# Performance work log

Measured on AMD Instinct MI355X. Metric: run time of the kernel, lower is better.

Reference implementation:

```python
import jax, jax.numpy as jnp
import numpy as np

B, T, C, H = 4, 2048, 1024, 16
HS = C // H  # 64
THRESH_INIT = (5 + 1) / 12 * 0.01  # (layer_idx+1)/n_layer * final_token_threshold


def _layernorm(x, w, b, eps=1e-5):
    mu = jnp.mean(x, axis=-1, keepdims=True)
    var = jnp.var(x, axis=-1, keepdims=True)
    return (x - mu) * jax.lax.rsqrt(var + eps) * w + b


def setup_inputs() -> dict:
    key = jax.random.key(0)
    ks = jax.random.split(key, 8)
    s = 0.02
    inp = {
        'x': jax.random.normal(ks[0], (B, T, C), dtype=jnp.float32),
        'attention_mask': jnp.ones((B, T), dtype=jnp.float32),
        'protected_mask': jnp.zeros((B, T), dtype=jnp.float32),
        'ln1_w': jnp.ones((C,), jnp.float32),
        'ln1_b': jnp.zeros((C,), jnp.float32),
        'c_attn_w': jax.random.normal(ks[1], (3 * C, C), jnp.float32) * s,
        'c_attn_b': jnp.zeros((3 * C,), jnp.float32),
        'c_proj_w': jax.random.normal(ks[2], (C, C), jnp.float32) * s,
        'c_proj_b': jnp.zeros((C,), jnp.float32),
        'ln2_w': jnp.ones((C,), jnp.float32),
        'ln2_b': jnp.zeros((C,), jnp.float32),
        'fc_w': jax.random.normal(ks[3], (4 * C, C), jnp.float32) * s,
        'fc_b': jnp.zeros((4 * C,), jnp.float32),
        'fcproj_w': jax.random.normal(ks[4], (C, 4 * C), jnp.float32) * s,
        'fcproj_b': jnp.zeros((C,), jnp.float32),
        'threshold': jnp.asarray(THRESH_INIT, jnp.float32),
    }
    return inp


def reference(x, attention_mask, protected_mask, ln1_w, ln1_b, c_attn_w, c_attn_b,
              c_proj_w, c_proj_b, ln2_w, ln2_b, fc_w, fc_b, fcproj_w, fcproj_b, threshold):
    b, t, c = x.shape
    # --- attention with importance scores ---
    h = _layernorm(x, ln1_w, ln1_b)
    qkv = h @ c_attn_w.T + c_attn_b                      # (B,T,3C)
    q, k, v = jnp.split(qkv, 3, axis=-1)
    q = q.reshape(b, t, H, HS).transpose(0, 2, 1, 3)     # (B,H,T,hs)
    k = k.reshape(b, t, H, HS).transpose(0, 2, 1, 3)
    v = v.reshape(b, t, H, HS).transpose(0, 2, 1, 3)
    att = jnp.einsum('bhqd,bhkd->bhqk', q, k) / np.sqrt(HS)
    causal = jnp.tril(jnp.ones((t, t), dtype=bool))      # (T,T)
    att = jnp.where(causal[None, None], att, -jnp.inf)
    att = jnp.where(attention_mask[:, None, None, :] != 0, att, -jnp.inf)
    att = jax.nn.softmax(att, axis=-1)                   # (B,H,T,T)
    y = jnp.einsum('bhqk,bhkd->bhqd', att, v)
    y = y.transpose(0, 2, 1, 3).reshape(b, t, c)
    y = y @ c_proj_w.T + c_proj_b
    importance = att.mean(axis=1).mean(axis=1)           # (B,T): mean over heads, then queries
    # --- pruning ---
    x = x + y
    pruning_mask = (importance >= threshold).astype(x.dtype)  # hard mode
    pruning_mask = jnp.where(protected_mask > 0, jnp.ones_like(pruning_mask), pruning_mask)
    combined_mask = attention_mask * pruning_mask
    x = x * combined_mask[..., None]
    # --- MLP ---
    m = _layernorm(x, ln2_w, ln2_b)
    m = jax.nn.gelu(m @ fc_w.T + fc_b, approximate=False)
    x = x + (m @ fcproj_w.T + fcproj_b)
    pruning_loss = jnp.asarray(0.0, x.dtype)  # hard mode / lambda=0
    return (x, combined_mask, pruning_loss)
```

## Files before the change

kernel.cpp:

```cpp
#include <hip/hip_runtime.h>
#include <math.h>

#define B_ 4
#define T_ 2048
#define C_ 1024
#define H_ 16
#define NROWS (B_*T_)

typedef short s8v  __attribute__((ext_vector_type(8)));
typedef float f4v  __attribute__((ext_vector_type(4)));
typedef unsigned short u16v4 __attribute__((ext_vector_type(4)));

static __device__ __forceinline__ unsigned short f2bf(float x) {
    unsigned u = __float_as_uint(x);
    unsigned r = u + 0x7fffu + ((u >> 16) & 1u);
    return (unsigned short)(r >> 16);
}

static __device__ __forceinline__ void gload_lds16(const void* g, void* l) {
    __builtin_amdgcn_global_load_lds(
        (const __attribute__((address_space(1))) void*)g,
        (__attribute__((address_space(3))) void*)l, 16, 0, 0);
}

__global__ __launch_bounds__(256) void ln_bf16(const float* __restrict__ x,
        const float* __restrict__ w, const float* __restrict__ b,
        unsigned short* __restrict__ out, const int* __restrict__ flag)
{
    if (flag && flag[0] == 0) return;
    int row = blockIdx.x;
    int tid = threadIdx.x;
    const float4* xr = (const float4*)(x + (size_t)row * C_);
    float4 v = xr[tid];
    float s  = v.x + v.y + v.z + v.w;
    float ss = v.x*v.x + v.y*v.y + v.z*v.z + v.w*v.w;
    #pragma unroll
    for (int off = 32; off > 0; off >>= 1) {
        s  += __shfl_down(s,  off, 64);
        ss += __shfl_down(ss, off, 64);
    }
    __shared__ float rs[4], rss[4];
    __shared__ float smu, srstd;
    int wave = tid >> 6, lane = tid & 63;
    if (lane == 0) { rs[wave] = s; rss[wave] = ss; }
    __syncthreads();
    if (tid == 0) {
        float S  = rs[0]+rs[1]+rs[2]+rs[3];
        float SS = rss[0]+rss[1]+rss[2]+rss[3];
        float mu = S * (1.0f/C_);
        float var = SS * (1.0f/C_) - mu*mu;
        smu = mu; srstd = rsqrtf(var + 1e-5f);
    }
    __syncthreads();
    float mu = smu, rstd = srstd;
    float4 wv = ((const float4*)w)[tid];
    float4 bv = ((const float4*)b)[tid];
    u16v4 o;
    o.x = f2bf((v.x-mu)*rstd*wv.x + bv.x);
    o.y = f2bf((v.y-mu)*rstd*wv.y + bv.y);
    o.z = f2bf((v.z-mu)*rstd*wv.z + bv.z);
    o.w = f2bf((v.w-mu)*rstd*wv.w + bv.w);
    *(u16v4*)(out + (size_t)row * C_ + tid*4) = o;
}

__global__ __launch_bounds__(256) void cvt_bf16(const float* __restrict__ in,
        unsigned short* __restrict__ out, int n4, const int* __restrict__ flag)
{
    if (flag && flag[0] == 0) return;
    int i = blockIdx.x * 256 + threadIdx.x;
    if (i < n4) {
        float4 v = ((const float4*)in)[i];
        u16v4 o = { f2bf(v.x), f2bf(v.y), f2bf(v.z), f2bf(v.w) };
        *(u16v4*)(out + (size_t)i*4) = o;
    }
}

__global__ __launch_bounds__(256) void cvt3_bf16(
        const float* __restrict__ cprojw, const float* __restrict__ fcw,
        const float* __restrict__ fcpw,
        unsigned short* __restrict__ wproj, unsigned short* __restrict__ wfc,
        unsigned short* __restrict__ wfcp, const int* __restrict__ flag)
{
    if (flag[0] == 0) return;
    int i = blockIdx.x * 256 + threadIdx.x;
    const int n1 = C_*C_/4;
    const int n2 = n1 + C_*C_;
    const float* src; unsigned short* dst; int j;
    if (i < n1)      { src = cprojw; dst = wproj; j = i; }
    else if (i < n2) { src = fcw;    dst = wfc;   j = i - n1; }
    else             { src = fcpw;   dst = wfcp;  j = i - n2; }
    float4 v = ((const float4*)src)[j];
    u16v4 o = { f2bf(v.x), f2bf(v.y), f2bf(v.z), f2bf(v.w) };
    *(u16v4*)(dst + (size_t)j*4) = o;
}

__global__ void zero_kernel(float* p, int n) {
    int i = blockIdx.x * 256 + threadIdx.x;
    if (i < n) p[i] = 0.f;
}

template<int EPI>
__global__ __launch_bounds__(256) void gemm_bf16(
    const unsigned short* __restrict__ A,
    const unsigned short* __restrict__ Bw,
    const float* __restrict__ bias,
    const float* __restrict__ res,
    float* __restrict__ Cout, unsigned short* __restrict__ Cbf,
    int K, int lda, int ldb, int ldc, int ncoff,
    const float* __restrict__ cmv,
    unsigned short* __restrict__ qh, unsigned short* __restrict__ kh,
    unsigned short* __restrict__ vh, const int* __restrict__ flag)
{
    if (flag && flag[0] == 0) return;
    __shared__ unsigned short As[128*64];
    __shared__ unsigned short Bs[128*64];
    int tid = threadIdx.x;
    int w = tid >> 6, lane = tid & 63, quad = lane >> 4, l16 = lane & 15;
    int wr = w >> 1, wc = w & 1;
    int m0 = blockIdx.y * 128, n0 = blockIdx.x * 128;

    size_t offA[4], offB[4];
    #pragma unroll
    for (int j = 0; j < 4; j++) {
        int ci = j*256 + tid;
        int mr = ci >> 3, kcs = ci & 7;
        int kc = kcs ^ (mr & 7);
        offA[j] = (size_t)(m0 + mr) * lda + kc*8;
        offB[j] = (size_t)(n0 + mr) * ldb + kc*8;
    }

    f4v acc[4][4];
    #pragma unroll
    for (int i = 0; i < 4; i++)
        #pragma unroll
        for (int j = 0; j < 4; j++) { acc[i][j][0]=0.f; acc[i][j][1]=0.f; acc[i][j][2]=0.f; acc[i][j][3]=0.f; }

    for (int k0 = 0; k0 < K; k0 += 64) {
        __syncthreads();
        #pragma unroll
        for (int j = 0; j < 4; j++) {
            gload_lds16(A  + offA[j] + k0, &As[(j*256 + (w<<6))*8]);
            gload_lds16(Bw + offB[j] + k0, &Bs[(j*256 + (w<<6))*8]);
        }
        __syncthreads();
        #pragma unroll
        for (int c = 0; c < 2; c++) {
            s8v af[4], bf[4];
            int sw = ((c<<2) + quad) ^ (l16 & 7);
            #pragma unroll
            for (int i = 0; i < 4; i++) {
                int mr = wr*64 + i*16 + l16;
                af[i] = *(const s8v*)&As[mr*64 + sw*8];
                int nr = wc*64 + i*16 + l16;
                bf[i] = *(const s8v*)&Bs[nr*64 + sw*8];
            }
            #pragma unroll
            for (int i = 0; i < 4; i++)
                #pragma unroll
                for (int j = 0; j < 4; j++)
                    acc[i][j] = __builtin_amdgcn_mfma_f32_16x16x32_bf16(af[i], bf[j], acc[i][j], 0, 0, 0);
        }
    }

    #pragma unroll
    for (int j = 0; j < 4; j++) {
        int ncol = n0 + wc*64 + j*16 + l16;
        float bv = bias ? bias[ncol] : 0.f;
        int hh = 0, dd = 0;
        bool qsec = false;
        unsigned short* basep = nullptr;
        if (EPI == 3) {
            int ncolg = ncol + ncoff;
            int sec = ncolg >> 10;
            int hn = ncolg & 1023;
            hh = hn >> 6; dd = hn & 63;
            basep = (sec == 0) ? qh : (sec == 1) ? kh : vh;
            qsec = (sec == 0);
        }
        #pragma unroll
        for (int i = 0; i < 4; i++) {
            #pragma unroll
            for (int reg = 0; reg < 4; reg++) {
                int m = m0 + wr*64 + i*16 + quad*4 + reg;
                float v = acc[i][j][reg] + bv;
                if (EPI == 1) {
                    v = 0.5f * v * (1.0f + erff(v * 0.70710678118654752f));
                    Cbf[(size_t)m*ldc + ncol] = f2bf(v);
                } else if (EPI == 2) {
                    Cout[(size_t)m*ldc + ncol] = v + res[(size_t)m*ldc + ncol];
                } else if (EPI == 3) {
                    if (qsec) v *= 0.125f;
                    int bb = m >> 11, t = m & 2047;
                    basep[(((size_t)(bb*H_ + hh))*T_ + t)*64 + dd] = f2bf(v);
                } else if (EPI == 4) {
                    Cout[(size_t)m*ldc + ncol] = (res[(size_t)m*ldc + ncol] + v) * cmv[m];
                }
            }
        }
    }
}

__global__ __launch_bounds__(256) void attn_imp(
    const unsigned short* __restrict__ qh, const unsigned short* __restrict__ kh,
    const float* __restrict__ amask, float* __restrict__ imp)
{
    __shared__ unsigned short Ks[2][64*64];
    __shared__ float msk01[2048];
    __shared__ float tileAll[32];
    __shared__ float colws[2][64];

    int tid = threadIdx.x;
    int w = tid >> 6, lane = tid & 63, quad = lane >> 4, l16 = lane & 15;
    int bh = blockIdx.x & 63;
    int pp = blockIdx.x >> 6;
    int b  = bh >> 4;
    int qtf[4] = { pp, 31 - pp, pp + 8, 23 - pp };
    int ntiles = 32 - pp;

    const unsigned short* qp = qh + (size_t)bh*T_*64;
    const unsigned short* kp = kh + (size_t)bh*T_*64;
    const float* amp = amask + b*T_;

    for (int i = tid; i < ntiles*64; i += 256)
        msk01[i] = (amp[i] != 0.f) ? 1.f : 0.f;
    if (tid < 128) colws[tid >> 6][tid & 63] = 0.f;
    __syncthreads();
    for (int t = w; t < ntiles; t += 4) {
        bool a = __all(msk01[t*64 + lane] != 0.f);
        if (lane == 0) tileAll[t] = a ? 1.f : 0.f;
    }

    int q0f[4];
    s8v aQ[4][2];
    #pragma unroll
    for (int f = 0; f < 4; f++) {
        q0f[f] = qtf[f]*64 + 16*w;
        aQ[f][0] = *(const s8v*)(qp + (size_t)(q0f[f] + l16)*64 + quad*8);
        aQ[f][1] = *(const s8v*)(qp + (size_t)(q0f[f] + l16)*64 + 32 + quad*8);
    }

    int r0 = tid >> 3,         c0 = (tid & 7) ^ (r0 & 7);
    int r1 = (256 + tid) >> 3, c1 = ((256 + tid) & 7) ^ (r1 & 7);

    float lrow[4][4];
    #pragma unroll
    for (int f = 0; f < 4; f++)
        #pragma unroll
        for (int reg = 0; reg < 4; reg++) lrow[f][reg] = 0.f;

    gload_lds16(kp + ((size_t)r0*64 + c0*8), &Ks[0][(w*64)*8]);
    gload_lds16(kp + ((size_t)r1*64 + c1*8), &Ks[0][(256 + w*64)*8]);

    for (int it = 0; it < ntiles; ++it) {
        __syncthreads();
        if (it + 1 < ntiles) {
            int kn = (it+1)*64, bufn = (it+1) & 1;
            gload_lds16(kp + ((size_t)(kn+r0)*64 + c0*8), &Ks[bufn][(w*64)*8]);
            gload_lds16(kp + ((size_t)(kn+r1)*64 + c1*8), &Ks[bufn][(256 + w*64)*8]);
        }
        const unsigned short* ks = Ks[it & 1];
        float allm = tileAll[it];
        float mk[4];
        #pragma unroll
        for (int nt = 0; nt < 4; nt++) mk[nt] = msk01[it*64 + nt*16 + l16];
        s8v bkr[2][4];
        #pragma unroll
        for (int c = 0; c < 2; c++)
            #pragma unroll
            for (int nt = 0; nt < 4; nt++)
                bkr[c][nt] = *(const s8v*)&ks[((nt*16 + l16)*8 + ((((c<<2)+quad) ^ (l16 & 7))))*8];

        #pragma unroll
        for (int f = 0; f < 4; f++) {
            if (it > qtf[f]) continue;
            f4v accS[4];
            #pragma unroll
            for (int nt = 0; nt < 4; nt++) { accS[nt][0]=0.f; accS[nt][1]=0.f; accS[nt][2]=0.f; accS[nt][3]=0.f; }
            #pragma unroll
            for (int c = 0; c < 2; c++)
                #pragma unroll
                for (int nt = 0; nt < 4; nt++)
                    accS[nt] = __builtin_amdgcn_mfma_f32_16x16x32_bf16(aQ[f][c], bkr[c][nt], accS[nt], 0, 0, 0);
            if (it < qtf[f] && allm != 0.f) {
                #pragma unroll
                for (int nt = 0; nt < 4; nt++)
                    #pragma unroll
                    for (int reg = 0; reg < 4; reg++)
                        lrow[f][reg] += __expf(accS[nt][reg]);
            } else {
                #pragma unroll
                for (int nt = 0; nt < 4; nt++) {
                    int kg = it*64 + nt*16 + l16;
                    #pragma unroll
                    for (int reg = 0; reg < 4; reg++) {
                        float me = (kg <= q0f[f] + quad*4 + reg) ? mk[nt] : 0.f;
                        lrow[f][reg] += __expf(accS[nt][reg]) * me;
                    }
                }
            }
        }
    }

    float linv[4][4];
    #pragma unroll
    for (int f = 0; f < 4; f++)
        #pragma unroll
        for (int reg = 0; reg < 4; reg++) {
            float v = lrow[f][reg];
            v += __shfl_xor(v, 1); v += __shfl_xor(v, 2);
            v += __shfl_xor(v, 4); v += __shfl_xor(v, 8);
            linv[f][reg] = (v > 0.f) ? 1.0f / v : 0.f;
        }

    __syncthreads();
    gload_lds16(kp + ((size_t)r0*64 + c0*8), &Ks[0][(w*64)*8]);
    gload_lds16(kp + ((size_t)r1*64 + c1*8), &Ks[0][(256 + w*64)*8]);

    for (int it = 0; it < ntiles; ++it) {
        __syncthreads();
        if (it + 1 < ntiles) {
            int kn = (it+1)*64, bufn = (it+1) & 1;
            gload_lds16(kp + ((size_t)(kn+r0)*64 + c0*8), &Ks[bufn][(w*64)*8]);
            gload_lds16(kp + ((size_t)(kn+r1)*64 + c1*8), &Ks[bufn][(256 + w*64)*8]);
        }
        if (it > 0 && tid < 64) {
            int ob = (it-1) & 1;
            atomicAdd(&imp[b*T_ + (it-1)*64 + tid], colws[ob][tid]);
            colws[ob][tid] = 0.f;
        }
        const unsigned short* ks = Ks[it & 1];
        float allm = tileAll[it];
        float mk[4];
        #pragma unroll
        for (int nt = 0; nt < 4; nt++) mk[nt] = msk01[it*64 + nt*16 + l16];
        s8v bkr[2][4];
        #pragma unroll
        for (int c = 0; c < 2; c++)
            #pragma unroll
            for (int nt = 0; nt < 4; nt++)
                bkr[c][nt] = *(const s8v*)&ks[((nt*16 + l16)*8 + ((((c<<2)+quad) ^ (l16 & 7))))*8];

        float cs[4] = {0.f, 0.f, 0.f, 0.f};
        #pragma unroll
        for (int f = 0; f < 4; f++) {
            if (it > qtf[f]) continue;
            f4v accS[4];
            #pragma unroll
            for (int nt = 0; nt < 4; nt++) { accS[nt][0]=0.f; accS[nt][1]=0.f; accS[nt][2]=0.f; accS[nt][3]=0.f; }
            #pragma unroll
            for (int c = 0; c < 2; c++)
                #pragma unroll
                for (int nt = 0; nt < 4; nt++)
                    accS[nt] = __builtin_amdgcn_mfma_f32_16x16x32_bf16(aQ[f][c], bkr[c][nt], accS[nt], 0, 0, 0);
            if (it < qtf[f] && allm != 0.f) {
                #pragma unroll
                for (int nt = 0; nt < 4; nt++)
                    #pragma unroll
                    for (int reg = 0; reg < 4; reg++)
                        cs[nt] += __expf(accS[nt][reg]) * linv[f][reg];
            } else {
                #pragma unroll
                for (int nt = 0; nt < 4; nt++) {
                    int kg = it*64 + nt*16 + l16;
                    #pragma unroll
                    for (int reg = 0; reg < 4; reg++) {
                        float me = (kg <= q0f[f] + quad*4 + reg) ? mk[nt] : 0.f;
                        cs[nt] += __expf(accS[nt][reg]) * linv[f][reg] * me;
                    }
                }
            }
        }
        #pragma unroll
        for (int nt = 0; nt < 4; nt++) {
            float v = cs[nt];
            v += __shfl_xor(v, 16);
            v += __shfl_xor(v, 32);
            if (quad == 0) atomicAdd(&colws[it & 1][nt*16 + l16], v);
        }
    }
    __syncthreads();
    if (tid < 64) atomicAdd(&imp[b*T_ + (ntiles-1)*64 + tid], colws[(ntiles-1) & 1][tid]);
}

__global__ __launch_bounds__(256) void mask_finalize(
    const float* __restrict__ imp, const float* __restrict__ amask,
    const float* __restrict__ prot, const float* __restrict__ thr,
    float* __restrict__ mask_out, float* __restrict__ loss_out,
    int* __restrict__ nsurv)
{
    int i = blockIdx.x * 256 + threadIdx.x;
    float impv = imp[i] * (1.0f / (float)(H_ * T_));
    float pm = (impv >= thr[0]) ? 1.f : 0.f;
    if (prot[i] > 0.f) pm = 1.f;
    float cm = amask[i] * pm;
    mask_out[i] = cm;
    if (i == 0) loss_out[0] = 0.f;
    unsigned long long bal = __ballot(cm != 0.f);
    int cnt = __popcll(bal);
    __shared__ int bs;
    if (threadIdx.x == 0) bs = 0;
    __syncthreads();
    if ((threadIdx.x & 63) == 0 && cnt) atomicAdd(&bs, cnt);
    __syncthreads();
    if (threadIdx.x == 0 && bs) atomicAdd(nsurv, bs);
}

__global__ __launch_bounds__(256) void attn_full(
    const unsigned short* __restrict__ qh, const unsigned short* __restrict__ kh,
    const unsigned short* __restrict__ vh, const float* __restrict__ amask,
    unsigned short* __restrict__ y, const int* __restrict__ flag)
{
    if (flag[0] == 0) return;
    __shared__ unsigned short Ks[64][72];
    __shared__ unsigned short Vt[64][72];
    __shared__ unsigned short Ps[4][16][72];
    __shared__ float mks[64];

    int tid = threadIdx.x;
    int w = tid >> 6, lane = tid & 63, quad = lane >> 4, l16 = lane & 15;
    int nqt = T_ / 64;
    int qt = blockIdx.x % nqt;
    int bh = blockIdx.x / nqt;
    int b = bh >> 4, h = bh & 15;
    int q0 = qt * 64;

    const unsigned short* qp = qh + (size_t)bh * T_ * 64;
    const unsigned short* kp = kh + (size_t)bh * T_ * 64;
    const unsigned short* vp = vh + (size_t)bh * T_ * 64;

    int qrow = q0 + 16*w + l16;
    s8v aQ0 = *(const s8v*)(qp + (size_t)qrow*64 + quad*8);
    s8v aQ1 = *(const s8v*)(qp + (size_t)qrow*64 + 32 + quad*8);

    int qwmax = q0 + 16*w + 15;
    int ntiles = qt + 1;
    int qg = q0 + 16*w + quad*4;

    float lrow[4] = {0.f, 0.f, 0.f, 0.f};
    for (int it = 0; it < ntiles; ++it) {
        int k0 = it * 64;
        __syncthreads();
        for (int cid = tid; cid < 512; cid += 256) {
            int row = cid >> 3, ch = cid & 7;
            *(s8v*)&Ks[row][ch*8] = *(const s8v*)(kp + (size_t)(k0+row)*64 + ch*8);
        }
        if (tid < 64) mks[tid] = amask[b*T_ + k0 + tid];
        __syncthreads();
        if (k0 > qwmax) continue;
        f4v accS[4];
        #pragma unroll
        for (int nt = 0; nt < 4; nt++) { accS[nt][0]=0.f; accS[nt][1]=0.f; accS[nt][2]=0.f; accS[nt][3]=0.f; }
        #pragma unroll
        for (int nt = 0; nt < 4; nt++) {
            s8v b0 = *(const s8v*)&Ks[nt*16 + l16][quad*8];
            s8v b1 = *(const s8v*)&Ks[nt*16 + l16][32 + quad*8];
            accS[nt] = __builtin_amdgcn_mfma_f32_16x16x32_bf16(aQ0, b0, accS[nt], 0, 0, 0);
            accS[nt] = __builtin_amdgcn_mfma_f32_16x16x32_bf16(aQ1, b1, accS[nt], 0, 0, 0);
        }
        #pragma unroll
        for (int nt = 0; nt < 4; nt++) {
            int kg = k0 + nt*16 + l16;
            float mkv = mks[nt*16 + l16];
            #pragma unroll
            for (int reg = 0; reg < 4; reg++) {
                bool val = (kg <= qg + reg) && (mkv != 0.f);
                float e = __expf(accS[nt][reg]);
                lrow[reg] += val ? e : 0.f;
            }
        }
    }
    float linv[4];
    #pragma unroll
    for (int reg = 0; reg < 4; reg++) {
        float v = lrow[reg];
        v += __shfl_xor(v, 1); v += __shfl_xor(v, 2);
        v += __shfl_xor(v, 4); v += __shfl_xor(v, 8);
        linv[reg] = (v > 0.f) ? 1.0f / v : 0.f;
    }

    f4v accO[4];
    #pragma unroll
    for (int nt = 0; nt < 4; nt++) { accO[nt][0]=0.f; accO[nt][1]=0.f; accO[nt][2]=0.f; accO[nt][3]=0.f; }

    for (int it = 0; it < ntiles; ++it) {
        int k0 = it * 64;
        __syncthreads();
        for (int cid = tid; cid < 512; cid += 256) {
            int row = cid >> 3, ch = cid & 7;
            s8v kv = *(const s8v*)(kp + (size_t)(k0+row)*64 + ch*8);
            *(s8v*)&Ks[row][ch*8] = kv;
            s8v vv = *(const s8v*)(vp + (size_t)(k0+row)*64 + ch*8);
            #pragma unroll
            for (int j = 0; j < 8; j++) Vt[ch*8 + j][row] = (unsigned short)vv[j];
        }
        if (tid < 64) mks[tid] = amask[b*T_ + k0 + tid];
        __syncthreads();
        if (k0 > qwmax) continue;
        f4v accS[4];
        #pragma unroll
        for (int nt = 0; nt < 4; nt++) { accS[nt][0]=0.f; accS[nt][1]=0.f; accS[nt][2]=0.f; accS[nt][3]=0.f; }
        #pragma unroll
        for (int nt = 0; nt < 4; nt++) {
            s8v b0 = *(const s8v*)&Ks[nt*16 + l16][quad*8];
            s8v b1 = *(const s8v*)&Ks[nt*16 + l16][32 + quad*8];
            accS[nt] = __builtin_amdgcn_mfma_f32_16x16x32_bf16(aQ0, b0, accS[nt], 0, 0, 0);
            accS[nt] = __builtin_amdgcn_mfma_f32_16x16x32_bf16(aQ1, b1, accS[nt], 0, 0, 0);
        }
        #pragma unroll
        for (int nt = 0; nt < 4; nt++) {
            int kg = k0 + nt*16 + l16;
            float mkv = mks[nt*16 + l16];
            #pragma unroll
            for (int reg = 0; reg < 4; reg++) {
                bool val = (kg <= qg + reg) && (mkv != 0.f);
                float p = val ? __expf(accS[nt][reg]) * linv[reg] : 0.f;
                Ps[w][quad*4 + reg][nt*16 + l16] = f2bf(p);
            }
        }
        s8v aP0 = *(const s8v*)&Ps[w][l16][quad*8];
        s8v aP1 = *(const s8v*)&Ps[w][l16][32 + quad*8];
        #pragma unroll
        for (int nt = 0; nt < 4; nt++) {
            s8v bv0 = *(const s8v*)&Vt[nt*16 + l16][quad*8];
            s8v bv1 = *(const s8v*)&Vt[nt*16 + l16][32 + quad*8];
            accO[nt] = __builtin_amdgcn_mfma_f32_16x16x32_bf16(aP0, bv0, accO[nt], 0, 0, 0);
            accO[nt] = __builtin_amdgcn_mfma_f32_16x16x32_bf16(aP1, bv1, accO[nt], 0, 0, 0);
        }
    }
    #pragma unroll
    for (int nt = 0; nt < 4; nt++) {
        #pragma unroll
        for (int reg = 0; reg < 4; reg++) {
            int q = q0 + 16*w + quad*4 + reg;
            y[((size_t)(b*T_ + q))*C_ + h*64 + nt*16 + l16] = f2bf(accO[nt][reg]);
        }
    }
}

__global__ __launch_bounds__(256) void ap_fc(const int* __restrict__ nsurv,
        const float* __restrict__ ln2b, const float* __restrict__ fcw,
        const float* __restrict__ fcb, float* __restrict__ abuf)
{
    if (nsurv[0] != 0) return;
    int j = blockIdx.x * 4 + (threadIdx.x >> 6);
    int lane = threadIdx.x & 63;
    const float* wr = fcw + (size_t)j * C_;
    float s = 0.f;
    for (int k = lane; k < C_; k += 64) s += ln2b[k] * wr[k];
    #pragma unroll
    for (int off = 32; off > 0; off >>= 1) s += __shfl_down(s, off, 64);
    if (lane == 0) {
        float v = fcb[j] + s;
        abuf[j] = 0.5f * v * (1.0f + erff(v * 0.70710678118654752f));
    }
}

__global__ __launch_bounds__(256) void ap_fcp(const int* __restrict__ nsurv,
        const float* __restrict__ abuf, const float* __restrict__ fcpw,
        const float* __restrict__ fcpb, float* __restrict__ rowbuf)
{
    if (nsurv[0] != 0) return;
    int c = blockIdx.x * 4 + (threadIdx.x >> 6);
    int lane = threadIdx.x & 63;
    const float* wr = fcpw + (size_t)c * (4*C_);
    float s = 0.f;
    for (int k = lane; k < 4*C_; k += 64) s += abuf[k] * wr[k];
    #pragma unroll
    for (int off = 32; off > 0; off >>= 1) s += __shfl_down(s, off, 64);
    if (lane == 0) rowbuf[c] = fcpb[c] + s;
}

__global__ __launch_bounds__(256) void ap_bcast(const int* __restrict__ nsurv,
        const float* __restrict__ rowbuf, float* __restrict__ out_x)
{
    if (nsurv[0] != 0) return;
    int r = blockIdx.x;
    float4 v = ((const float4*)rowbuf)[threadIdx.x];
    ((float4*)(out_x + (size_t)r * C_))[threadIdx.x] = v;
}

extern "C" void kernel_launch(void* const* d_in, const int* in_sizes, int n_in,
                              void* d_out, int out_size, void* d_ws, size_t ws_size,
                              hipStream_t stream) {
    const float* x       = (const float*)d_in[0];
    const float* amask   = (const float*)d_in[1];
    const float* prot    = (const float*)d_in[2];
    const float* ln1w    = (const float*)d_in[3];
    const float* ln1b    = (const float*)d_in[4];
    const float* cattn_w = (const float*)d_in[5];
    const float* cattn_b = (const float*)d_in[6];
    const float* cproj_w = (const float*)d_in[7];
    const float* cproj_b = (const float*)d_in[8];
    const float* ln2w    = (const float*)d_in[9];
    const float* ln2b    = (const float*)d_in[10];
    const float* fcw     = (const float*)d_in[11];
    const float* fcb     = (const float*)d_in[12];
    const float* fcpw    = (const float*)d_in[13];
    const float* fcpb    = (const float*)d_in[14];
    const float* thr     = (const float*)d_in[15];

    unsigned short* wqkv  = (unsigned short*)d_ws;
    unsigned short* wproj = wqkv  + (size_t)3*C_*C_;
    unsigned short* wfc   = wproj + (size_t)C_*C_;
    unsigned short* wfcp  = wfc   + (size_t)4*C_*C_;
    unsigned short* hbuf  = wfcp  + (size_t)4*C_*C_;
    unsigned short* qh    = hbuf  + (size_t)NROWS*C_;
    unsigned short* kh    = qh    + (size_t)NROWS*C_;
    unsigned short* vh    = kh    + (size_t)NROWS*C_;
    unsigned short* cbuf  = qh;
    float* imp    = (float*)(vh + (size_t)NROWS*C_);
    int*   nsurv  = (int*)(imp + NROWS);
    float* abuf   = (float*)(nsurv + 4);
    float* rowbuf = abuf + 4*C_;

    float* out_x    = (float*)d_out;
    float* out_mask = out_x + (size_t)NROWS*C_;
    float* out_loss = out_mask + NROWS;

    hipLaunchKernelGGL(zero_kernel, dim3((NROWS+8+255)/256), dim3(256), 0, stream,
                       imp, NROWS + 4);
    hipLaunchKernelGGL(cvt_bf16, dim3(3*C_*C_/4/256), dim3(256), 0, stream,
                       cattn_w, wqkv, 3*C_*C_/4, nullptr);
    hipLaunchKernelGGL(ln_bf16, dim3(NROWS), dim3(256), 0, stream, x, ln1w, ln1b, hbuf, nullptr);
    hipLaunchKernelGGL((gemm_bf16<3>), dim3(2048/128, NROWS/128), dim3(256), 0, stream,
                       hbuf, wqkv, cattn_b, nullptr, nullptr, nullptr,
                       C_, C_, C_, 0, 0, nullptr, qh, kh, vh, nullptr);
    hipLaunchKernelGGL(attn_imp, dim3(64*8), dim3(256), 0, stream, qh, kh, amask, imp);
    hipLaunchKernelGGL(mask_finalize, dim3(NROWS/256), dim3(256), 0, stream,
                       imp, amask, prot, thr, out_mask, out_loss, nsurv);

    hipLaunchKernelGGL(cvt3_bf16, dim3(9*C_*C_/4/256), dim3(256), 0, stream,
                       cproj_w, fcw, fcpw, wproj, wfc, wfcp, nsurv);
    hipLaunchKernelGGL((gemm_bf16<3>), dim3(1024/128, NROWS/128), dim3(256), 0, stream,
                       hbuf, wqkv + (size_t)2048*C_, cattn_b + 2048, nullptr, nullptr, nullptr,
                       C_, C_, C_, 0, 2048, nullptr, qh, kh, vh, nsurv);
    hipLaunchKernelGGL(attn_full, dim3(B_*H_*(T_/64)), dim3(256), 0, stream,
                       qh, kh, vh, amask, hbuf, nsurv);
    hipLaunchKernelGGL((gemm_bf16<4>), dim3(C_/128, NROWS/128), dim3(256), 0, stream,
                       hbuf, wproj, cproj_b, x, out_x, nullptr,
                       C_, C_, C_, C_, 0, out_mask, nullptr, nullptr, nullptr, nsurv);
    hipLaunchKernelGGL(ln_bf16, dim3(NROWS), dim3(256), 0, stream, out_x, ln2w, ln2b, hbuf, nsurv);
    for (int j = 0; j < 2; j++) {
        hipLaunchKernelGGL((gemm_bf16<1>), dim3(2048/128, NROWS/128), dim3(256), 0, stream,
                           hbuf, wfc + (size_t)j*2048*C_, fcb + j*2048, nullptr, nullptr, cbuf,
                           C_, C_, C_, 2048, 0, nullptr, nullptr, nullptr, nullptr, nsurv);
        hipLaunchKernelGGL((gemm_bf16<2>), dim3(C_/128, NROWS/128), dim3(256), 0, stream,
                           cbuf, wfcp + (size_t)j*2048, (j == 0) ? fcpb : nullptr, out_x, out_x, nullptr,
                           2048, 2048, 4*C_, C_, 0, nullptr, nullptr, nullptr, nullptr, nsurv);
    }

    hipLaunchKernelGGL(ap_fc,    dim3(4*C_/4), dim3(256), 0, stream, nsurv, ln2b, fcw, fcb, abuf);
    hipLaunchKernelGGL(ap_fcp,   dim3(C_/4),   dim3(256), 0, stream, nsurv, abuf, fcpw, fcpb, rowbuf);
    hipLaunchKernelGGL(ap_bcast, dim3(NROWS),  dim3(256), 0, stream, nsurv, rowbuf, out_x);
}
```

Before: 352.4 us.

## Split importance attention into row-sum and column-sum kernels with exp2 scaling

Replaces the single attn_imp kernel, which ran two passes over the keys with LDS double buffering across 512 blocks, with two kernels. attn_rowsum computes per-query softmax normalisers into a buffer, and attn_colsum computes column sums per key tile over 2048 blocks with waves splitting the tiles. The Q scale now folds in log2(e) so every exp becomes a hardware exp2, including inside attn_full. This gives more parallelism and better load balance, at the cost of a second launch, an extra linv buffer round trip through global memory, and K/Q reads straight from global memory without LDS staging.

```diff
diff --git a/kernel.cpp b/kernel.cpp
--- a/kernel.cpp
+++ b/kernel.cpp
@@ -11,10 +11,16 @@
 typedef float f4v  __attribute__((ext_vector_type(4)));
 typedef unsigned short u16v4 __attribute__((ext_vector_type(4)));
 
+#define QSCALE 0.1803368801111f
+
 static __device__ __forceinline__ unsigned short f2bf(float x) {
     unsigned u = __float_as_uint(x);
     unsigned r = u + 0x7fffu + ((u >> 16) & 1u);
     return (unsigned short)(r >> 16);
+}
+
+static __device__ __forceinline__ float fexp2(float x) {
+    return __builtin_amdgcn_exp2f(x);
 }
 
 static __device__ __forceinline__ void gload_lds16(const void* g, void* l) {
@@ -189,7 +195,7 @@
                 } else if (EPI == 2) {
                     Cout[(size_t)m*ldc + ncol] = v + res[(size_t)m*ldc + ncol];
                 } else if (EPI == 3) {
-                    if (qsec) v *= 0.125f;
+                    if (qsec) v *= QSCALE;
                     int bb = m >> 11, t = m & 2047;
                     basep[(((size_t)(bb*H_ + hh))*T_ + t)*64 + dd] = f2bf(v);
                 } else if (EPI == 4) {
@@ -200,22 +206,20 @@
     }
 }
 
-__global__ __launch_bounds__(256) void attn_imp(
+__global__ __launch_bounds__(256) void attn_rowsum(
     const unsigned short* __restrict__ qh, const unsigned short* __restrict__ kh,
-    const float* __restrict__ amask, float* __restrict__ imp)
-{
-    __shared__ unsigned short Ks[2][64*64];
+    const float* __restrict__ amask, float* __restrict__ linvbuf)
+{
     __shared__ float msk01[2048];
-    __shared__ float tileAll[32];
-    __shared__ float colws[2][64];
+    __shared__ float lred[4][64];
 
     int tid = threadIdx.x;
     int w = tid >> 6, lane = tid & 63, quad = lane >> 4, l16 = lane & 15;
+    int qt = 31 - (blockIdx.x >> 6);
     int bh = blockIdx.x & 63;
-    int pp = blockIdx.x >> 6;
     int b  = bh >> 4;
-    int qtf[4] = { pp, 31 - pp, pp + 8, 23 - pp };
-    int ntiles = 32 - pp;
+    int q0 = qt * 64;
+    int ntiles = qt + 1;
 
     const unsigned short* qp = qh + (size_t)bh*T_*64;
     const unsigned short* kp = kh + (size_t)bh*T_*64;
@@ -223,163 +227,172 @@
 
     for (int i = tid; i < ntiles*64; i += 256)
         msk01[i] = (amp[i] != 0.f) ? 1.f : 0.f;
-    if (tid < 128) colws[tid >> 6][tid & 63] = 0.f;
     __syncthreads();
-    for (int t = w; t < ntiles; t += 4) {
-        bool a = __all(msk01[t*64 + lane] != 0.f);
-        if (lane == 0) tileAll[t] = a ? 1.f : 0.f;
-    }
-
-    int q0f[4];
+
     s8v aQ[4][2];
     #pragma unroll
-    for (int f = 0; f < 4; f++) {
-        q0f[f] = qtf[f]*64 + 16*w;
-        aQ[f][0] = *(const s8v*)(qp + (size_t)(q0f[f] + l16)*64 + quad*8);
-        aQ[f][1] = *(const s8v*)(qp + (size_t)(q0f[f] + l16)*64 + 32 + quad*8);
-    }
-
-    int r0 = tid >> 3,         c0 = (tid & 7) ^ (r0 & 7);
-    int r1 = (256 + tid) >> 3, c1 = ((256 + tid) & 7) ^ (r1 & 7);
+    for (int qf = 0; qf < 4; qf++) {
+        int row = q0 + qf*16 + l16;
+        aQ[qf][0] = *(const s8v*)(qp + (size_t)row*64 + quad*8);
+        aQ[qf][1] = *(const s8v*)(qp + (size_t)row*64 + 32 + quad*8);
+    }
 
     float lrow[4][4];
     #pragma unroll
-    for (int f = 0; f < 4; f++)
-        #pragma unroll
-        for (int reg = 0; reg < 4; reg++) lrow[f][reg] = 0.f;
-
-    gload_lds16(kp + ((size_t)r0*64 + c0*8), &Ks[0][(w*64)*8]);
-    gload_lds16(kp + ((size_t)r1*64 + c1*8), &Ks[0][(256 + w*64)*8]);
-
-    for (int it = 0; it < ntiles; ++it) {
-        __syncthreads();
-        if (it + 1 < ntiles) {
-            int kn = (it+1)*64, bufn = (it+1) & 1;
-            gload_lds16(kp + ((size_t)(kn+r0)*64 + c0*8), &Ks[bufn][(w*64)*8]);
-            gload_lds16(kp + ((size_t)(kn+r1)*64 + c1*8), &Ks[bufn][(256 + w*64)*8]);
-        }
-        const unsigned short* ks = Ks[it & 1];
-        float allm = tileAll[it];
+    for (int qf = 0; qf < 4; qf++)
+        #pragma unroll
+        for (int reg = 0; reg < 4; reg++) lrow[qf][reg] = 0.f;
+
+    for (int it = w; it < ntiles; it += 4) {
+        int k0 = it * 64;
+        s8v bk[2][4];
+        #pragma unroll
+        for (int c = 0; c < 2; c++)
+            #pragma unroll
+            for (int nt = 0; nt < 4; nt++)
+                bk[c][nt] = *(const s8v*)(kp + (size_t)(k0 + nt*16 + l16)*64 + c*32 + quad*8);
         float mk[4];
         #pragma unroll
-        for (int nt = 0; nt < 4; nt++) mk[nt] = msk01[it*64 + nt*16 + l16];
-        s8v bkr[2][4];
-        #pragma unroll
-        for (int c = 0; c < 2; c++)
-            #pragma unroll
-            for (int nt = 0; nt < 4; nt++)
-                bkr[c][nt] = *(const s8v*)&ks[((nt*16 + l16)*8 + ((((c<<2)+quad) ^ (l16 & 7))))*8];
-
-        #pragma unroll
-        for (int f = 0; f < 4; f++) {
-            if (it > qtf[f]) continue;
-            f4v accS[4];
-            #pragma unroll
-            for (int nt = 0; nt < 4; nt++) { accS[nt][0]=0.f; accS[nt][1]=0.f; accS[nt][2]=0.f; accS[nt][3]=0.f; }
+        for (int nt = 0; nt < 4; nt++) mk[nt] = msk01[k0 + nt*16 + l16];
+        bool allm = __all(mk[0] != 0.f && mk[1] != 0.f && mk[2] != 0.f && mk[3] != 0.f);
+
+        #pragma unroll
+        for (int qf = 0; qf < 4; qf++) {
+            f4v acc[4];
+            #pragma unroll
+            for (int nt = 0; nt < 4; nt++) { acc[nt][0]=0.f; acc[nt][1]=0.f; acc[nt][2]=0.f; acc[nt][3]=0.f; }
             #pragma unroll
             for (int c = 0; c < 2; c++)
                 #pragma unroll
                 for (int nt = 0; nt < 4; nt++)
-                    accS[nt] = __builtin_amdgcn_mfma_f32_16x16x32_bf16(aQ[f][c], bkr[c][nt], accS[nt], 0, 0, 0);
-            if (it < qtf[f] && allm != 0.f) {
+                    acc[nt] = __builtin_amdgcn_mfma_f32_16x16x32_bf16(aQ[qf][c], bk[c][nt], acc[nt], 0, 0, 0);
+            if (it < qt && allm) {
                 #pragma unroll
                 for (int nt = 0; nt < 4; nt++)
                     #pragma unroll
                     for (int reg = 0; reg < 4; reg++)
-                        lrow[f][reg] += __expf(accS[nt][reg]);
-            } else {
-                #pragma unroll
-                for (int nt = 0; nt < 4; nt++) {
-                    int kg = it*64 + nt*16 + l16;
-                    #pragma unroll
-                    for (int reg = 0; reg < 4; reg++) {
-                        float me = (kg <= q0f[f] + quad*4 + reg) ? mk[nt] : 0.f;
-                        lrow[f][reg] += __expf(accS[nt][reg]) * me;
-                    }
-                }
-            }
-        }
-    }
-
-    float linv[4][4];
-    #pragma unroll
-    for (int f = 0; f < 4; f++)
-        #pragma unroll
-        for (int reg = 0; reg < 4; reg++) {
-            float v = lrow[f][reg];
-            v += __shfl_xor(v, 1); v += __shfl_xor(v, 2);
-            v += __shfl_xor(v, 4); v += __shfl_xor(v, 8);
-            linv[f][reg] = (v > 0.f) ? 1.0f / v : 0.f;
-        }
-
-    __syncthreads();
-    gload_lds16(kp + ((size_t)r0*64 + c0*8), &Ks[0][(w*64)*8]);
-    gload_lds16(kp + ((size_t)r1*64 + c1*8), &Ks[0][(256 + w*64)*8]);
-
-    for (int it = 0; it < ntiles; ++it) {
-        __syncthreads();
-        if (it + 1 < ntiles) {
-            int kn = (it+1)*64, bufn = (it+1) & 1;
-            gload_lds16(kp + ((size_t)(kn+r0)*64 + c0*8), &Ks[bufn][(w*64)*8]);
-            gload_lds16(kp + ((size_t)(kn+r1)*64 + c1*8), &Ks[bufn][(256 + w*64)*8]);
-        }
-        if (it > 0 && tid < 64) {
-            int ob = (it-1) & 1;
-            atomicAdd(&imp[b*T_ + (it-1)*64 + tid], colws[ob][tid]);
-            colws[ob][tid] = 0.f;
-        }
-        const unsigned short* ks = Ks[it & 1];
-        float allm = tileAll[it];
-        float mk[4];
-        #pragma unroll
-        for (int nt = 0; nt < 4; nt++) mk[nt] = msk01[it*64 + nt*16 + l16];
-        s8v bkr[2][4];
-        #pragma unroll
-        for (int c = 0; c < 2; c++)
-            #pragma unroll
-            for (int nt = 0; nt < 4; nt++)
-                bkr[c][nt] = *(const s8v*)&ks[((nt*16 + l16)*8 + ((((c<<2)+quad) ^ (l16 & 7))))*8];
-
-        float cs[4] = {0.f, 0.f, 0.f, 0.f};
-        #pragma unroll
-        for (int f = 0; f < 4; f++) {
-            if (it > qtf[f]) continue;
-            f4v accS[4];
-            #pragma unroll
-            for (int nt = 0; nt < 4; nt++) { accS[nt][0]=0.f; accS[nt][1]=0.f; accS[nt][2]=0.f; accS[nt][3]=0.f; }
-            #pragma unroll
-            for (int c = 0; c < 2; c++)
-                #pragma unroll
-                for (int nt = 0; nt < 4; nt++)
-                    accS[nt] = __builtin_amdgcn_mfma_f32_16x16x32_bf16(aQ[f][c], bkr[c][nt], accS[nt], 0, 0, 0);
-            if (it < qtf[f] && allm != 0.f) {
+                        lrow[qf][reg] += fexp2(acc[nt][reg]);
+            } else if (it < qt) {
                 #pragma unroll
                 for (int nt = 0; nt < 4; nt++)
                     #pragma unroll
                     for (int reg = 0; reg < 4; reg++)
-                        cs[nt] += __expf(accS[nt][reg]) * linv[f][reg];
+                        lrow[qf][reg] += fexp2(acc[nt][reg]) * mk[nt];
             } else {
                 #pragma unroll
                 for (int nt = 0; nt < 4; nt++) {
-                    int kg = it*64 + nt*16 + l16;
+                    int kg = k0 + nt*16 + l16;
                     #pragma unroll
                     for (int reg = 0; reg < 4; reg++) {
-                        float me = (kg <= q0f[f] + quad*4 + reg) ? mk[nt] : 0.f;
-                        cs[nt] += __expf(accS[nt][reg]) * linv[f][reg] * me;
+                        float me = (kg <= q0 + qf*16 + quad*4 + reg) ? mk[nt] : 0.f;
+                        lrow[qf][reg] += fexp2(acc[nt][reg]) * me;
                     }
                 }
             }
         }
-        #pragma unroll
-        for (int nt = 0; nt < 4; nt++) {
-            float v = cs[nt];
-            v += __shfl_xor(v, 16);
-            v += __shfl_xor(v, 32);
-            if (quad == 0) atomicAdd(&colws[it & 1][nt*16 + l16], v);
-        }
+    }
+
+    #pragma unroll
+    for (int qf = 0; qf < 4; qf++)
+        #pragma unroll
+        for (int reg = 0; reg < 4; reg++) {
+            float v = lrow[qf][reg];
+            v += __shfl_xor(v, 1); v += __shfl_xor(v, 2);
+            v += __shfl_xor(v, 4); v += __shfl_xor(v, 8);
+            lrow[qf][reg] = v;
+        }
+    if (l16 == 0) {
+        #pragma unroll
+        for (int qf = 0; qf < 4; qf++)
+            #pragma unroll
+            for (int reg = 0; reg < 4; reg++)
+                lred[w][qf*16 + quad*4 + reg] = lrow[qf][reg];
     }
     __syncthreads();
-    if (tid < 64) atomicAdd(&imp[b*T_ + (ntiles-1)*64 + tid], colws[(ntiles-1) & 1][tid]);
+    if (tid < 64) {
+        float t = lred[0][tid] + lred[1][tid] + lred[2][tid] + lred[3][tid];
+        linvbuf[(size_t)bh*T_ + q0 + tid] = (t > 0.f) ? 1.0f / t : 0.f;
+    }
+}
+
+__global__ __launch_bounds__(256) void attn_colsum(
+    const unsigned short* __restrict__ qh, const unsigned short* __restrict__ kh,
+    const float* __restrict__ amask, const float* __restrict__ linvbuf,
+    float* __restrict__ imp)
+{
+    __shared__ float cred[4][64];
+
+    int tid = threadIdx.x;
+    int w = tid >> 6, lane = tid & 63, quad = lane >> 4, l16 = lane & 15;
+    int kc = blockIdx.x >> 6;
+    int bh = blockIdx.x & 63;
+    int b  = bh >> 4;
+    int k0 = kc * 64;
+
+    const unsigned short* qp = qh + (size_t)bh*T_*64;
+    const unsigned short* kp = kh + (size_t)bh*T_*64;
+    const float* lp = linvbuf + (size_t)bh*T_;
+
+    s8v bk[2][4];
+    float mk[4];
+    #pragma unroll
+    for (int nt = 0; nt < 4; nt++) {
+        int key = k0 + nt*16 + l16;
+        bk[0][nt] = *(const s8v*)(kp + (size_t)key*64 + quad*8);
+        bk[1][nt] = *(const s8v*)(kp + (size_t)key*64 + 32 + quad*8);
+        mk[nt] = amask[b*T_ + key];
+    }
+
+    float cs[4] = {0.f, 0.f, 0.f, 0.f};
+
+    for (int qt = kc + w; qt < 32; qt += 4) {
+        int q0 = qt * 64;
+        #pragma unroll
+        for (int qf = 0; qf < 4; qf++) {
+            int row = q0 + qf*16 + l16;
+            s8v a0 = *(const s8v*)(qp + (size_t)row*64 + quad*8);
+            s8v a1 = *(const s8v*)(qp + (size_t)row*64 + 32 + quad*8);
+            float4 linv4 = *(const float4*)(lp + q0 + qf*16 + quad*4);
+            f4v acc[4];
+            #pragma unroll
+            for (int nt = 0; nt < 4; nt++) { acc[nt][0]=0.f; acc[nt][1]=0.f; acc[nt][2]=0.f; acc[nt][3]=0.f; }
+            #pragma unroll
+            for (int nt = 0; nt < 4; nt++) {
+                acc[nt] = __builtin_amdgcn_mfma_f32_16x16x32_bf16(a0, bk[0][nt], acc[nt], 0, 0, 0);
+                acc[nt] = __builtin_amdgcn_mfma_f32_16x16x32_bf16(a1, bk[1][nt], acc[nt], 0, 0, 0);
+            }
+            float lv[4] = { linv4.x, linv4.y, linv4.z, linv4.w };
+            if (qt > kc) {
+                #pragma unroll
+                for (int nt = 0; nt < 4; nt++)
+                    #pragma unroll
+                    for (int reg = 0; reg < 4; reg++)
+                        cs[nt] += fexp2(acc[nt][reg]) * lv[reg];
+            } else {
+                #pragma unroll
+                for (int nt = 0; nt < 4; nt++) {
+                    int kg = k0 + nt*16 + l16;
+                    #pragma unroll
+                    for (int reg = 0; reg < 4; reg++) {
+                        float me = (kg <= q0 + qf*16 + quad*4 + reg) ? 1.f : 0.f;
+                        cs[nt] += fexp2(acc[nt][reg]) * lv[reg] * me;
+                    }
+                }
+            }
+        }
+    }
+
+    #pragma unroll
+    for (int nt = 0; nt < 4; nt++) {
+        float v = cs[nt] * mk[nt];
+        v += __shfl_xor(v, 16);
+        v += __shfl_xor(v, 32);
+        if (quad == 0) cred[w][nt*16 + l16] = v;
+    }
+    __syncthreads();
+    if (tid < 64)
+        atomicAdd(&imp[b*T_ + k0 + tid],
+                  cred[0][tid] + cred[1][tid] + cred[2][tid] + cred[3][tid]);
 }
 
 __global__ __launch_bounds__(256) void mask_finalize(
@@ -464,7 +477,7 @@
             #pragma unroll
             for (int reg = 0; reg < 4; reg++) {
                 bool val = (kg <= qg + reg) && (mkv != 0.f);
-                float e = __expf(accS[nt][reg]);
+                float e = fexp2(accS[nt][reg]);
                 lrow[reg] += val ? e : 0.f;
             }
         }
@@ -513,7 +526,7 @@
             #pragma unroll
             for (int reg = 0; reg < 4; reg++) {
                 bool val = (kg <= qg + reg) && (mkv != 0.f);
-                float p = val ? __expf(accS[nt][reg]) * linv[reg] : 0.f;
+                float p = val ? fexp2(accS[nt][reg]) * linv[reg] : 0.f;
                 Ps[w][quad*4 + reg][nt*16 + l16] = f2bf(p);
             }
         }
@@ -612,6 +625,7 @@
     int*   nsurv  = (int*)(imp + NROWS);
     float* abuf   = (float*)(nsurv + 4);
     float* rowbuf = abuf + 4*C_;
+    float* linvbuf = rowbuf + C_;
 
     float* out_x    = (float*)d_out;
     float* out_mask = out_x + (size_t)NROWS*C_;
@@ -625,7 +639,10 @@
     hipLaunchKernelGGL((gemm_bf16<3>), dim3(2048/128, NROWS/128), dim3(256), 0, stream,
                        hbuf, wqkv, cattn_b, nullptr, nullptr, nullptr,
                        C_, C_, C_, 0, 0, nullptr, qh, kh, vh, nullptr);
-    hipLaunchKernelGGL(attn_imp, dim3(64*8), dim3(256), 0, stream, qh, kh, amask, imp);
+    hipLaunchKernelGGL(attn_rowsum, dim3(64*32), dim3(256), 0, stream,
+                       qh, kh, amask, linvbuf);
+    hipLaunchKernelGGL(attn_colsum, dim3(64*32), dim3(256), 0, stream,
+                       qh, kh, amask, linvbuf, imp);
     hipLaunchKernelGGL(mask_finalize, dim3(NROWS/256), dim3(256), 0, stream,
                        imp, amask, prot, thr, out_mask, out_loss, nsurv);
 
```

After: 348.2 us. No clear change (-1.2%).
